# Kernel optimization log

Measured on AMD Instinct MI355X. Metric: run time of the kernel, lower is better.

Reference implementation:

```python
import jax, jax.numpy as jnp
import numpy as np

N = 50000   # nodes
E = 512000  # edges
D = 64      # embedding_dim
L = 4       # num_layers
ATOM_DIMS = np.array([119, 5, 12, 12, 10, 6, 6, 2, 2])  # OGB atom feature vocab sizes
BOND_DIMS = np.array([5, 6, 2])                          # OGB bond feature vocab sizes


def _ln(x, g, b, eps=1e-5):
    m = x.mean(-1, keepdims=True)
    v = x.var(-1, keepdims=True)
    return (x - m) * jax.lax.rsqrt(v + eps) * g + b


def setup_inputs() -> dict:
    key = jax.random.key(0)
    ks = jax.random.split(key, 12)
    s = 0.05
    x = jax.random.randint(ks[0], (N, 9), 0, jnp.asarray(ATOM_DIMS)[None, :])
    edge_attr = jax.random.randint(ks[1], (E, 3), 0, jnp.asarray(BOND_DIMS)[None, :])
    edge_index = jax.random.randint(ks[2], (2, E), 0, N)
    # padded embedding tables: [n_feats, max_vocab, D]
    atom_emb = jax.random.normal(ks[3], (9, 119, D), jnp.float32) * s
    bond_emb = jax.random.normal(ks[4], (3, 6, D), jnp.float32) * s
    eps = jnp.zeros((L,), jnp.float32)  # GIN eps, init 0
    W1 = jax.random.normal(ks[5], (L, D, 2 * D), jnp.float32) * s
    b1 = jnp.zeros((L, 2 * D), jnp.float32)
    W2 = jax.random.normal(ks[6], (L, 2 * D, D), jnp.float32) * s
    b2 = jnp.zeros((L, D), jnp.float32)
    ln_g = jnp.ones((L, D), jnp.float32)
    ln_b = jnp.zeros((L, D), jnp.float32)
    Wu1 = jax.random.normal(ks[7], (L, 3 * D, 3 * D), jnp.float32) * s
    bu1 = jnp.zeros((L, 3 * D), jnp.float32)
    ug = jnp.ones((L, 3 * D), jnp.float32)
    ub = jnp.zeros((L, 3 * D), jnp.float32)
    Wu2 = jax.random.normal(ks[8], (L, 3 * D, D), jnp.float32) * s
    bu2 = jnp.zeros((L, D), jnp.float32)
    return dict(x=x, edge_attr=edge_attr, edge_index=edge_index,
                atom_emb=atom_emb, bond_emb=bond_emb, eps=eps,
                W1=W1, b1=b1, W2=W2, b2=b2, ln_g=ln_g, ln_b=ln_b,
                Wu1=Wu1, bu1=bu1, ug=ug, ub=ub, Wu2=Wu2, bu2=bu2)


def reference(x, edge_attr, edge_index, atom_emb, bond_emb, eps,
              W1, b1, W2, b2, ln_g, ln_b, Wu1, bu1, ug, ub, Wu2, bu2):
    # Atom/Bond encoders: sum of per-column categorical embeddings
    node = atom_emb[jnp.arange(9)[None, :], x].sum(axis=1)       # [N, D]
    edge = bond_emb[jnp.arange(3)[None, :], edge_attr].sum(axis=1)  # [E, D]
    src, dst = edge_index[0], edge_index[1]
    for l in range(L):
        # MyGINConv (GINE): aggregate relu(x_src + e) at dst, mlp((1+eps)x + agg)
        msg = jax.nn.relu(node[src] + edge)                      # [E, D]
        agg = jax.ops.segment_sum(msg, dst, num_segments=N)      # [N, D]
        h = (1.0 + eps[l]) * node + agg
        h = jax.nn.relu(h @ W1[l] + b1[l]) @ W2[l] + b2[l]       # conv MLP
        h = _ln(h, ln_g[l], ln_b[l])                             # batch_norms[l] (LayerNorm)
        node = jax.nn.relu(h) + node                             # dropout=identity (eval) + residual
        # SparseEdgeUpdateLayer (residual=True)
        cat = jnp.concatenate([node[src], node[dst], edge], axis=-1)  # [E, 3D]
        m = _ln(cat @ Wu1[l] + bu1[l], ug[l], ub[l])
        edge = jax.nn.relu(m) @ Wu2[l] + bu2[l] + edge
    return node, edge
```

## Files before the change

kernel.cpp:

```cpp
#include <hip/hip_runtime.h>
#include <hip/hip_bf16.h>


#define GIN_N 50000
#define GIN_E 512000

typedef __attribute__((ext_vector_type(8))) short short8;
typedef __attribute__((ext_vector_type(4))) short short4v;
typedef __attribute__((ext_vector_type(4))) float f32x4;
typedef unsigned short u16;

__device__ __forceinline__ u16 bf16r(float x) {
    unsigned u = __builtin_bit_cast(unsigned, x);
    u += 0x7fffu + ((u >> 16) & 1u);
    return (u16)(u >> 16);
}
__device__ __forceinline__ float bf16f(u16 h) {
    unsigned u = ((unsigned)h) << 16;
    return __builtin_bit_cast(float, u);
}

__global__ __launch_bounds__(256) void zero_f32(float* __restrict__ p, int n) {
    int i = blockIdx.x * 256 + threadIdx.x;
    if (i < n) p[i] = 0.f;
}
__global__ __launch_bounds__(256) void zero_i32(int* __restrict__ p, int n) {
    int i = blockIdx.x * 256 + threadIdx.x;
    if (i < n) p[i] = 0;
}

__global__ __launch_bounds__(256) void atom_encode(const int* __restrict__ x,
        const float* __restrict__ emb, float* __restrict__ node, int N) {
    int idx = blockIdx.x * 256 + threadIdx.x;
    int n = idx >> 6, lane = idx & 63;
    if (n >= N) return;
    float s = 0.f;
#pragma unroll
    for (int f = 0; f < 9; ++f) {
        int v = x[n * 9 + f];
        s += emb[(f * 119 + v) * 64 + lane];
    }
    node[(size_t)n * 64 + lane] = s;
}

__global__ __launch_bounds__(256) void csr_hist(const int* __restrict__ dst,
                                                int* __restrict__ deg, int E) {
    int e = blockIdx.x * 256 + threadIdx.x;
    if (e < E) atomicAdd(&deg[dst[e]], 1);
}
__global__ __launch_bounds__(1024) void csr_scan(const int* __restrict__ deg,
                                                 int* __restrict__ cursor, int N) {
    __shared__ int ps[1024];
    const int t = threadIdx.x;
    const int chunk = (N + 1023) / 1024;
    const int base = t * chunk;
    int s = 0;
    for (int i = 0; i < chunk; ++i) {
        int idx = base + i;
        if (idx < N) s += deg[idx];
    }
    ps[t] = s;
    __syncthreads();
    for (int off = 1; off < 1024; off <<= 1) {
        int v = (t >= off) ? ps[t - off] : 0;
        __syncthreads();
        ps[t] += v;
        __syncthreads();
    }
    int run = ps[t] - s;
    for (int i = 0; i < chunk; ++i) {
        int idx = base + i;
        if (idx < N) { cursor[idx] = run; run += deg[idx]; }
    }
}
__global__ __launch_bounds__(256) void csr_fill(const int* __restrict__ src,
        const int* __restrict__ dst, int* __restrict__ cursor,
        int* __restrict__ perm, int* __restrict__ srcS, int* __restrict__ dstS,
        int E) {
    int e = blockIdx.x * 256 + threadIdx.x;
    if (e < E) {
        int d = dst[e];
        int pos = atomicAdd(&cursor[d], 1);
        perm[pos] = e;
        srcS[pos] = src[e];
        dstS[pos] = d;
    }
}

__global__ __launch_bounds__(256) void bond_encode_seg(
        const int* __restrict__ ea, const float* __restrict__ emb,
        u16* __restrict__ edgeB, const int* __restrict__ perm,
        const int* __restrict__ srcS, const int* __restrict__ dstS,
        const float* __restrict__ node, float* __restrict__ agg) {
    __shared__ float msgF[64][66];
    __shared__ int dstL[64];
    const int t = threadIdx.x, w = t >> 6, lane = t & 63;
    const int tile = (blockIdx.x & 7) * (gridDim.x >> 3) + (blockIdx.x >> 3);
    const long eB = (long)tile * 64;

    if (t < 64) dstL[t] = dstS[eB + t];
#pragma unroll 1
    for (int i = 0; i < 16; ++i) {
        int r = w * 16 + i;
        long e = eB + r;
        int pe = perm[e];
        float s = 0.f;
#pragma unroll
        for (int f = 0; f < 3; ++f) {
            int v = ea[pe * 3 + f];
            s += emb[(f * 6 + v) * 64 + lane];
        }
        edgeB[(size_t)e * 64 + lane] = bf16r(s);
        int si = srcS[e];
        msgF[r][lane] = fmaxf(node[(size_t)si * 64 + lane] + s, 0.f);
    }
    __syncthreads();
    const int colR = t & 63;
    const int h = t >> 6;
    float acc = 0.f;
#pragma unroll 1
    for (int r = h * 16; r < h * 16 + 16; ++r) {
        acc += msgF[r][colR];
        if (r == h * 16 + 15 || dstL[r + 1] != dstL[r]) {
            unsafeAtomicAdd(&agg[(size_t)dstL[r] * 64 + colR], acc);
            acc = 0.f;
        }
    }
}

__global__ __launch_bounds__(256) void pack_b1(const float* __restrict__ W,
        u16* __restrict__ out, int K, int Nc, int F) {
    int tid = blockIdx.x * 256 + threadIdx.x;
    int lane = tid & 63;
    int frag = (tid >> 6) % F;
    int layer = tid / (F * 64);
    int tpr = Nc / 16;
    int ks = frag / tpr, tt = frag % tpr;
    int k0 = ks * 32 + ((lane >> 4) << 3);
    int col = tt * 16 + (lane & 15);
    const float* w = W + (size_t)layer * K * Nc;
    u16* o = out + ((size_t)layer * F + frag) * 512 + (size_t)lane * 8;
#pragma unroll
    for (int j = 0; j < 8; ++j) o[j] = bf16r(w[(size_t)(k0 + j) * Nc + col]);
}
__global__ __launch_bounds__(256) void pack_b2(const float* __restrict__ W,
        u16* __restrict__ out, int K, int Nc, int F) {
    int tid = blockIdx.x * 256 + threadIdx.x;
    int lane = tid & 63;
    int frag = (tid >> 6) % F;
    int layer = tid / (F * 64);
    int tpr = Nc / 16;
    int ks = frag / tpr, tt = frag % tpr;
    int k0 = ks * 32 + ((lane >> 4) << 3);
    int col = tt * 16 + (lane & 15);
    const float* w = W + (size_t)layer * K * Nc;
    u16* o = out + ((size_t)layer * F + frag) * 1024 + (size_t)lane * 8;
#pragma unroll
    for (int j = 0; j < 8; ++j) {
        float v = w[(size_t)(k0 + j) * Nc + col];
        u16 hi = bf16r(v);
        o[j] = hi;
        o[512 + j] = bf16r(v - bf16f(hi));
    }
}

__global__ __launch_bounds__(256, 2) void node_mlp(
        float* __restrict__ node, u16* __restrict__ nodeB,
        float* __restrict__ agg,
        const float* __restrict__ epsArr, int l,
        const u16* __restrict__ pw1, const u16* __restrict__ pw2,
        const float* __restrict__ b1, const float* __restrict__ b2,
        const float* __restrict__ lng, const float* __restrict__ lnb, int N) {
    __shared__ u16 xH[64][72], xL[64][72];
    __shared__ u16 hH[64][136], hL[64][136];
    __shared__ float pS[4][64], pS2[4][64], lnM[64], lnR[64];
    const int t = threadIdx.x, w = t >> 6, lane = t & 63;
    const int g = lane >> 4, c0 = lane & 15;
    const float epf = 1.f + epsArr[l];

#pragma unroll
    for (int i = 0; i < 16; ++i) {
        int r = w * 16 + i;
        int n = blockIdx.x * 64 + r;
        float x = 0.f;
        if (n < N) {
            size_t o = (size_t)n * 64 + lane;
            x = epf * node[o] + agg[o];
            agg[o] = 0.f;
        }
        u16 h = bf16r(x);
        xH[r][lane] = h;
        xL[r][lane] = bf16r(x - bf16f(h));
    }
    __syncthreads();

    f32x4 a1[4][2];
#pragma unroll
    for (int sp = 0; sp < 4; ++sp)
#pragma unroll
        for (int lt = 0; lt < 2; ++lt) a1[sp][lt] = (f32x4)0.f;
#pragma unroll
    for (int ks = 0; ks < 2; ++ks) {
        short8 aH[4], aL[4];
#pragma unroll
        for (int sp = 0; sp < 4; ++sp) {
            aH[sp] = *(const short8*)&xH[sp * 16 + c0][ks * 32 + g * 8];
            aL[sp] = *(const short8*)&xL[sp * 16 + c0][ks * 32 + g * 8];
        }
#pragma unroll
        for (int lt = 0; lt < 2; ++lt) {
            const u16* p = pw1 + (size_t)(ks * 8 + w * 2 + lt) * 1024 + (size_t)lane * 8;
            short8 bH = *(const short8*)p;
            short8 bL = *(const short8*)(p + 512);
#pragma unroll
            for (int sp = 0; sp < 4; ++sp) {
                a1[sp][lt] = __builtin_amdgcn_mfma_f32_16x16x32_bf16(aH[sp], bH, a1[sp][lt], 0, 0, 0);
                a1[sp][lt] = __builtin_amdgcn_mfma_f32_16x16x32_bf16(aH[sp], bL, a1[sp][lt], 0, 0, 0);
                a1[sp][lt] = __builtin_amdgcn_mfma_f32_16x16x32_bf16(aL[sp], bH, a1[sp][lt], 0, 0, 0);
            }
        }
    }
#pragma unroll
    for (int lt = 0; lt < 2; ++lt) {
        int col = w * 32 + lt * 16 + c0;
        float bias = b1[col];
#pragma unroll
        for (int sp = 0; sp < 4; ++sp)
#pragma unroll
            for (int rg = 0; rg < 4; ++rg) {
                int r = sp * 16 + g * 4 + rg;
                float v = fmaxf(a1[sp][lt][rg] + bias, 0.f);
                u16 h = bf16r(v);
                hH[r][col] = h;
                hL[r][col] = bf16r(v - bf16f(h));
            }
    }
    __syncthreads();

    f32x4 a2[4];
#pragma unroll
    for (int sp = 0; sp < 4; ++sp) a2[sp] = (f32x4)0.f;
#pragma unroll
    for (int ks = 0; ks < 4; ++ks) {
        const u16* p = pw2 + (size_t)(ks * 4 + w) * 1024 + (size_t)lane * 8;
        short8 bH = *(const short8*)p;
        short8 bL = *(const short8*)(p + 512);
#pragma unroll
        for (int sp = 0; sp < 4; ++sp) {
            short8 aH = *(const short8*)&hH[sp * 16 + c0][ks * 32 + g * 8];
            short8 aL = *(const short8*)&hL[sp * 16 + c0][ks * 32 + g * 8];
            a2[sp] = __builtin_amdgcn_mfma_f32_16x16x32_bf16(aH, bH, a2[sp], 0, 0, 0);
            a2[sp] = __builtin_amdgcn_mfma_f32_16x16x32_bf16(aH, bL, a2[sp], 0, 0, 0);
            a2[sp] = __builtin_amdgcn_mfma_f32_16x16x32_bf16(aL, bH, a2[sp], 0, 0, 0);
        }
    }
    float bias2 = b2[w * 16 + c0];
    float s1v[4][4], s2v[4][4];
#pragma unroll
    for (int sp = 0; sp < 4; ++sp)
#pragma unroll
        for (int rg = 0; rg < 4; ++rg) {
            float v = a2[sp][rg] + bias2;
            a2[sp][rg] = v;
            s1v[sp][rg] = v;
            s2v[sp][rg] = v * v;
        }
#pragma unroll
    for (int off = 1; off < 16; off <<= 1)
#pragma unroll
        for (int sp = 0; sp < 4; ++sp)
#pragma unroll
            for (int rg = 0; rg < 4; ++rg) {
                s1v[sp][rg] += __shfl_xor(s1v[sp][rg], off);
                s2v[sp][rg] += __shfl_xor(s2v[sp][rg], off);
            }
    if (c0 == 0) {
#pragma unroll
        for (int sp = 0; sp < 4; ++sp)
#pragma unroll
            for (int rg = 0; rg < 4; ++rg) {
                int r = sp * 16 + g * 4 + rg;
                pS[w][r] = s1v[sp][rg];
                pS2[w][r] = s2v[sp][rg];
            }
    }
    __syncthreads();
    if (t < 64) {
        float a = pS[0][t] + pS[1][t] + pS[2][t] + pS[3][t];
        float b = pS2[0][t] + pS2[1][t] + pS2[2][t] + pS2[3][t];
        float mean = a * (1.f / 64.f);
        float var = b * (1.f / 64.f) - mean * mean;
        lnM[t] = mean;
        lnR[t] = rsqrtf(var + 1e-5f);
    }
    __syncthreads();

    int col = w * 16 + c0;
    float gg = lng[col], bc = lnb[col];
#pragma unroll
    for (int sp = 0; sp < 4; ++sp)
#pragma unroll
        for (int rg = 0; rg < 4; ++rg) {
            int r = sp * 16 + g * 4 + rg;
            int n = blockIdx.x * 64 + r;
            if (n < N) {
                size_t o = (size_t)n * 64 + col;
                float y = (a2[sp][rg] - lnM[r]) * lnR[r] * gg + bc;
                float out = fmaxf(y, 0.f) + node[o];
                node[o] = out;
                nodeB[o] = bf16r(out);
            }
        }
}

template <bool SCATTER>
__global__ __launch_bounds__(256, 4) void edge_update_v9(
        const int* __restrict__ src, const int* __restrict__ dst,
        const int* __restrict__ perm,
        const float* __restrict__ node, const u16* __restrict__ nodeB,
        u16* __restrict__ edgeB, float* __restrict__ edgeF,
        float* __restrict__ agg,
        const u16* __restrict__ pb1, const u16* __restrict__ pb2,
        const float* __restrict__ bu1, const float* __restrict__ ug,
        const float* __restrict__ ub, const float* __restrict__ bu2) {
    __shared__ u16 cat[64][200];
    __shared__ float pS[4][64], pS2[4][64];
    __shared__ float lnM[64], lnR[64];
    __shared__ int dstL[64], srcL[64];
    const int t = threadIdx.x, w = t >> 6, lane = t & 63;
    const int g = lane >> 4, c0 = lane & 15;
    const int tile = (blockIdx.x & 7) * (gridDim.x >> 3) + (blockIdx.x >> 3);
    const long eB = (long)tile * 64;

    if (t < 64) { dstL[t] = dst[eB + t]; srcL[t] = src[eB + t]; }
#pragma unroll
    for (int i = 0; i < 16; ++i) {
        int r = w * 16 + i;
        long ge = eB + r;
        int s = src[ge], d = dst[ge];
        cat[r][lane]      = nodeB[(size_t)s * 64 + lane];
        cat[r][64 + lane] = nodeB[(size_t)d * 64 + lane];
    }
    {
        const u16* eTile = edgeB + (size_t)eB * 64;
#pragma unroll
        for (int q = 0; q < 4; ++q) {
            int gi = t + q * 256;
            int r = gi >> 4, c4 = (gi & 15) * 4;
            *(short4v*)&cat[r][128 + c4] = *(const short4v*)(eTile + gi * 4);
        }
    }
    __syncthreads();

    u16 eold16[16];
#pragma unroll
    for (int sp = 0; sp < 4; ++sp)
#pragma unroll
        for (int rg = 0; rg < 4; ++rg)
            eold16[sp * 4 + rg] = cat[sp * 16 + g * 4 + rg][128 + w * 16 + c0];

    f32x4 acc[4][3];
#pragma unroll
    for (int sp = 0; sp < 4; ++sp)
#pragma unroll
        for (int lt = 0; lt < 3; ++lt) acc[sp][lt] = (f32x4)0.f;
#pragma unroll
    for (int ks = 0; ks < 6; ++ks) {
        short8 a[4];
#pragma unroll
        for (int sp = 0; sp < 4; ++sp)
            a[sp] = *(const short8*)&cat[sp * 16 + c0][ks * 32 + g * 8];
#pragma unroll
        for (int lt = 0; lt < 3; ++lt) {
            const u16* p = pb1 + (size_t)(ks * 12 + w * 3 + lt) * 512 + (size_t)lane * 8;
            short8 b = *(const short8*)p;
#pragma unroll
            for (int sp = 0; sp < 4; ++sp)
                acc[sp][lt] = __builtin_amdgcn_mfma_f32_16x16x32_bf16(a[sp], b, acc[sp][lt], 0, 0, 0);
        }
    }

    float bs[3];
#pragma unroll
    for (int lt = 0; lt < 3; ++lt) bs[lt] = bu1[w * 48 + lt * 16 + c0];
    float s1v[4][4], s2v[4][4];
#pragma unroll
    for (int sp = 0; sp < 4; ++sp)
#pragma unroll
        for (int rg = 0; rg < 4; ++rg) { s1v[sp][rg] = 0.f; s2v[sp][rg] = 0.f; }
#pragma unroll
    for (int sp = 0; sp < 4; ++sp)
#pragma unroll
        for (int lt = 0; lt < 3; ++lt)
#pragma unroll
            for (int rg = 0; rg < 4; ++rg) {
                float v = acc[sp][lt][rg] + bs[lt];
                acc[sp][lt][rg] = v;
                s1v[sp][rg] += v;
                s2v[sp][rg] += v * v;
            }
#pragma unroll
    for (int off = 1; off < 16; off <<= 1)
#pragma unroll
        for (int sp = 0; sp < 4; ++sp)
#pragma unroll
            for (int rg = 0; rg < 4; ++rg) {
                s1v[sp][rg] += __shfl_xor(s1v[sp][rg], off);
                s2v[sp][rg] += __shfl_xor(s2v[sp][rg], off);
            }
    if (c0 == 0) {
#pragma unroll
        for (int sp = 0; sp < 4; ++sp)
#pragma unroll
            for (int rg = 0; rg < 4; ++rg) {
                int r = sp * 16 + g * 4 + rg;
                pS[w][r] = s1v[sp][rg];
                pS2[w][r] = s2v[sp][rg];
            }
    }
    __syncthreads();
    if (t < 64) {
        float a = pS[0][t] + pS[1][t] + pS[2][t] + pS[3][t];
        float b = pS2[0][t] + pS2[1][t] + pS2[2][t] + pS2[3][t];
        float mean = a * (1.f / 192.f);
        float var = b * (1.f / 192.f) - mean * mean;
        lnM[t] = mean;
        lnR[t] = rsqrtf(var + 1e-5f);
    }
    __syncthreads();

#pragma unroll
    for (int lt = 0; lt < 3; ++lt) {
        int col = w * 48 + lt * 16 + c0;
        float gg = ug[col], bb = ub[col];
#pragma unroll
        for (int sp = 0; sp < 4; ++sp)
#pragma unroll
            for (int rg = 0; rg < 4; ++rg) {
                int r = sp * 16 + g * 4 + rg;
                float v = (acc[sp][lt][rg] - lnM[r]) * lnR[r] * gg + bb;
                cat[r][col] = bf16r(fmaxf(v, 0.f));
            }
    }
    __syncthreads();

    f32x4 a2[4];
#pragma unroll
    for (int sp = 0; sp < 4; ++sp) a2[sp] = (f32x4)0.f;
#pragma unroll
    for (int ks = 0; ks < 6; ++ks) {
        const u16* p = pb2 + (size_t)(ks * 4 + w) * 512 + (size_t)lane * 8;
        short8 b = *(const short8*)p;
#pragma unroll
        for (int sp = 0; sp < 4; ++sp) {
            short8 a = *(const short8*)&cat[sp * 16 + c0][ks * 32 + g * 8];
            a2[sp] = __builtin_amdgcn_mfma_f32_16x16x32_bf16(a, b, a2[sp], 0, 0, 0);
        }
    }
    __syncthreads();

    float* msgF = (float*)&cat[0][0];
    const int col = w * 16 + c0;
    const float bb2 = bu2[col];
#pragma unroll
    for (int sp = 0; sp < 4; ++sp)
#pragma unroll
        for (int rg = 0; rg < 4; ++rg) {
            int r = sp * 16 + g * 4 + rg;
            long ge = eB + r;
            float eNew = a2[sp][rg] + bb2 + bf16f(eold16[sp * 4 + rg]);
            if (SCATTER) {
                edgeB[(size_t)ge * 64 + col] = bf16r(eNew);
                float msg = fmaxf(node[(size_t)srcL[r] * 64 + col] + eNew, 0.f);
                msgF[r * 66 + col] = msg;
            } else {
                edgeF[(size_t)perm[ge] * 64 + col] = eNew;
            }
        }

    if (SCATTER) {
        __syncthreads();
        const int colR = t & 63;
        const int h = t >> 6;
        float accm = 0.f;
#pragma unroll 1
        for (int r = h * 16; r < h * 16 + 16; ++r) {
            accm += msgF[r * 66 + colR];
            if (r == h * 16 + 15 || dstL[r + 1] != dstL[r]) {
                unsafeAtomicAdd(&agg[(size_t)dstL[r] * 64 + colR], accm);
                accm = 0.f;
            }
        }
    }
}

extern "C" void kernel_launch(void* const* d_in, const int* in_sizes, int n_in,
                              void* d_out, int out_size, void* d_ws, size_t ws_size,
                              hipStream_t stream) {
    const int*   x         = (const int*)d_in[0];
    const int*   edge_attr = (const int*)d_in[1];
    const int*   edge_index= (const int*)d_in[2];
    const float* atom_emb  = (const float*)d_in[3];
    const float* bond_emb  = (const float*)d_in[4];
    const float* eps       = (const float*)d_in[5];
    const float* W1        = (const float*)d_in[6];
    const float* b1        = (const float*)d_in[7];
    const float* W2        = (const float*)d_in[8];
    const float* b2        = (const float*)d_in[9];
    const float* ln_g      = (const float*)d_in[10];
    const float* ln_b      = (const float*)d_in[11];
    const float* Wu1       = (const float*)d_in[12];
    const float* bu1       = (const float*)d_in[13];
    const float* ug        = (const float*)d_in[14];
    const float* ub        = (const float*)d_in[15];
    const float* Wu2       = (const float*)d_in[16];
    const float* bu2       = (const float*)d_in[17];

    const int N = GIN_N, E = GIN_E;
    const int* src = edge_index;
    const int* dst = edge_index + E;

    float* node  = (float*)d_out;
    float* edgeF = (float*)d_out + (size_t)N * 64;

    char* ws = (char*)d_ws;
    float* agg   = (float*)ws;  ws += (size_t)N * 64 * 4;
    u16*   nodeB = (u16*)ws;    ws += (size_t)N * 64 * 2;
    u16*   edgeB = (u16*)ws;    ws += (size_t)E * 64 * 2;
    int*   perm  = (int*)ws;    ws += (size_t)E * 4;
    int*   srcS  = (int*)ws;    ws += (size_t)E * 4;
    int*   dstS  = (int*)ws;    ws += (size_t)E * 4;
    int*   deg   = (int*)ws;    ws += (size_t)N * 4;
    int*   cursor= (int*)ws;    ws += (size_t)(N + 1) * 4;
    u16* pb1     = (u16*)ws;    ws += (size_t)4 * 72 * 512 * 2;
    u16* pb2     = (u16*)ws;    ws += (size_t)4 * 24 * 512 * 2;
    u16* pw1     = (u16*)ws;    ws += (size_t)4 * 16 * 1024 * 2;
    u16* pw2     = (u16*)ws;    ws += (size_t)4 * 16 * 1024 * 2;

    pack_b1<<<(4 * 72 * 64) / 256, 256, 0, stream>>>(Wu1, pb1, 192, 192, 72);
    pack_b1<<<(4 * 24 * 64) / 256, 256, 0, stream>>>(Wu2, pb2, 192, 64, 24);
    pack_b2<<<(4 * 16 * 64) / 256, 256, 0, stream>>>(W1, pw1, 64, 128, 16);
    pack_b2<<<(4 * 16 * 64) / 256, 256, 0, stream>>>(W2, pw2, 128, 64, 16);

    zero_i32<<<(N + 255) / 256, 256, 0, stream>>>(deg, N);
    csr_hist<<<E / 256, 256, 0, stream>>>(dst, deg, E);
    csr_scan<<<1, 1024, 0, stream>>>(deg, cursor, N);
    csr_fill<<<E / 256, 256, 0, stream>>>(src, dst, cursor, perm, srcS, dstS, E);

    atom_encode<<<(N * 64 + 255) / 256, 256, 0, stream>>>(x, atom_emb, node, N);
    zero_f32<<<(N * 64) / 256, 256, 0, stream>>>(agg, N * 64);
    bond_encode_seg<<<E / 64, 256, 0, stream>>>(edge_attr, bond_emb,
        edgeB, perm, srcS, dstS, node, agg);

    const int nodeBlocks = (N + 63) / 64;
    for (int l = 0; l < 4; ++l) {
        node_mlp<<<nodeBlocks, 256, 0, stream>>>(node, nodeB, agg, eps, l,
            pw1 + (size_t)l * 16 * 1024, pw2 + (size_t)l * 16 * 1024,
            b1 + (size_t)l * 128, b2 + (size_t)l * 64,
            ln_g + (size_t)l * 64, ln_b + (size_t)l * 64, N);
        if (l < 3)
            edge_update_v9<true><<<E / 64, 256, 0, stream>>>(srcS, dstS, perm,
                node, nodeB, edgeB, edgeF, agg,
                pb1 + (size_t)l * 72 * 512, pb2 + (size_t)l * 24 * 512,
                bu1 + (size_t)l * 192,
                ug + (size_t)l * 192, ub + (size_t)l * 192,
                bu2 + (size_t)l * 64);
        else
            edge_update_v9<false><<<E / 64, 256, 0, stream>>>(srcS, dstS, perm,
                node, nodeB, edgeB, edgeF, agg,
                pb1 + (size_t)l * 72 * 512, pb2 + (size_t)l * 24 * 512,
                bu1 + (size_t)l * 192,
                ug + (size_t)l * 192, ub + (size_t)l * 192,
                bu2 + (size_t)l * 64);
    }
}
```

Baseline: 959.5 us.

## Replace atomic scatter aggregation with CSR gather over materialized messages

Edge kernels now write per-edge relu messages in dst-sorted order to a buffer (aliasing the edge output), and node_mlp sums each node's contiguous message range via a CSR rowptr instead of reading an atomically accumulated agg buffer. This removes the float atomics, the agg zeroing and its reset, plus the shared-memory segment reduction. In exchange each layer writes and re-reads a full E×64 fp32 message array, greatly increasing memory traffic, and node_mlp's load phase becomes a serial variable-length gather.

```diff
diff --git a/kernel.cpp b/kernel.cpp
--- a/kernel.cpp
+++ b/kernel.cpp
@@ -20,10 +20,6 @@
     return __builtin_bit_cast(float, u);
 }
 
-__global__ __launch_bounds__(256) void zero_f32(float* __restrict__ p, int n) {
-    int i = blockIdx.x * 256 + threadIdx.x;
-    if (i < n) p[i] = 0.f;
-}
 __global__ __launch_bounds__(256) void zero_i32(int* __restrict__ p, int n) {
     int i = blockIdx.x * 256 + threadIdx.x;
     if (i < n) p[i] = 0;
@@ -49,7 +45,7 @@
     if (e < E) atomicAdd(&deg[dst[e]], 1);
 }
 __global__ __launch_bounds__(1024) void csr_scan(const int* __restrict__ deg,
-                                                 int* __restrict__ cursor, int N) {
+        int* __restrict__ rowptr, int* __restrict__ cursor, int N, int E) {
     __shared__ int ps[1024];
     const int t = threadIdx.x;
     const int chunk = (N + 1023) / 1024;
@@ -70,8 +66,9 @@
     int run = ps[t] - s;
     for (int i = 0; i < chunk; ++i) {
         int idx = base + i;
-        if (idx < N) { cursor[idx] = run; run += deg[idx]; }
-    }
+        if (idx < N) { rowptr[idx] = run; cursor[idx] = run; run += deg[idx]; }
+    }
+    if (t == 1023) rowptr[N] = E;
 }
 __global__ __launch_bounds__(256) void csr_fill(const int* __restrict__ src,
         const int* __restrict__ dst, int* __restrict__ cursor,
@@ -87,45 +84,24 @@
     }
 }
 
-__global__ __launch_bounds__(256) void bond_encode_seg(
+__global__ __launch_bounds__(256) void bond_encode_sorted(
         const int* __restrict__ ea, const float* __restrict__ emb,
-        u16* __restrict__ edgeB, const int* __restrict__ perm,
-        const int* __restrict__ srcS, const int* __restrict__ dstS,
-        const float* __restrict__ node, float* __restrict__ agg) {
-    __shared__ float msgF[64][66];
-    __shared__ int dstL[64];
-    const int t = threadIdx.x, w = t >> 6, lane = t & 63;
-    const int tile = (blockIdx.x & 7) * (gridDim.x >> 3) + (blockIdx.x >> 3);
-    const long eB = (long)tile * 64;
-
-    if (t < 64) dstL[t] = dstS[eB + t];
-#pragma unroll 1
-    for (int i = 0; i < 16; ++i) {
-        int r = w * 16 + i;
-        long e = eB + r;
-        int pe = perm[e];
-        float s = 0.f;
-#pragma unroll
-        for (int f = 0; f < 3; ++f) {
-            int v = ea[pe * 3 + f];
-            s += emb[(f * 6 + v) * 64 + lane];
-        }
-        edgeB[(size_t)e * 64 + lane] = bf16r(s);
-        int si = srcS[e];
-        msgF[r][lane] = fmaxf(node[(size_t)si * 64 + lane] + s, 0.f);
-    }
-    __syncthreads();
-    const int colR = t & 63;
-    const int h = t >> 6;
-    float acc = 0.f;
-#pragma unroll 1
-    for (int r = h * 16; r < h * 16 + 16; ++r) {
-        acc += msgF[r][colR];
-        if (r == h * 16 + 15 || dstL[r + 1] != dstL[r]) {
-            unsafeAtomicAdd(&agg[(size_t)dstL[r] * 64 + colR], acc);
-            acc = 0.f;
-        }
-    }
+        u16* __restrict__ edgeB, float* __restrict__ msg,
+        const int* __restrict__ perm, const int* __restrict__ srcS,
+        const float* __restrict__ node, int E) {
+    int idx = blockIdx.x * 256 + threadIdx.x;
+    int e = idx >> 6, lane = idx & 63;
+    if (e >= E) return;
+    int pe = perm[e];
+    float s = 0.f;
+#pragma unroll
+    for (int f = 0; f < 3; ++f) {
+        int v = ea[pe * 3 + f];
+        s += emb[(f * 6 + v) * 64 + lane];
+    }
+    edgeB[(size_t)e * 64 + lane] = bf16r(s);
+    int si = srcS[e];
+    msg[(size_t)e * 64 + lane] = fmaxf(node[(size_t)si * 64 + lane] + s, 0.f);
 }
 
 __global__ __launch_bounds__(256) void pack_b1(const float* __restrict__ W,
@@ -166,7 +142,7 @@
 
 __global__ __launch_bounds__(256, 2) void node_mlp(
         float* __restrict__ node, u16* __restrict__ nodeB,
-        float* __restrict__ agg,
+        const float* __restrict__ msg, const int* __restrict__ rowptr,
         const float* __restrict__ epsArr, int l,
         const u16* __restrict__ pw1, const u16* __restrict__ pw2,
         const float* __restrict__ b1, const float* __restrict__ b2,
@@ -178,15 +154,24 @@
     const int g = lane >> 4, c0 = lane & 15;
     const float epf = 1.f + epsArr[l];
 
-#pragma unroll
+#pragma unroll 1
     for (int i = 0; i < 16; ++i) {
         int r = w * 16 + i;
         int n = blockIdx.x * 64 + r;
         float x = 0.f;
         if (n < N) {
+            int jb = rowptr[n], je = rowptr[n + 1];
+            float a0 = 0.f, a1 = 0.f, a2v = 0.f, a3 = 0.f;
+            int j = jb;
+            for (; j + 3 < je; j += 4) {
+                a0  += msg[(size_t)j * 64 + lane];
+                a1  += msg[(size_t)(j + 1) * 64 + lane];
+                a2v += msg[(size_t)(j + 2) * 64 + lane];
+                a3  += msg[(size_t)(j + 3) * 64 + lane];
+            }
+            for (; j < je; ++j) a0 += msg[(size_t)j * 64 + lane];
             size_t o = (size_t)n * 64 + lane;
-            x = epf * node[o] + agg[o];
-            agg[o] = 0.f;
+            x = epf * node[o] + ((a0 + a1) + (a2v + a3));
         }
         u16 h = bf16r(x);
         xH[r][lane] = h;
@@ -313,26 +298,25 @@
         }
 }
 
-template <bool SCATTER>
-__global__ __launch_bounds__(256, 4) void edge_update_v9(
+template <bool LAST>
+__global__ __launch_bounds__(256, 4) void edge_update_v11(
         const int* __restrict__ src, const int* __restrict__ dst,
         const int* __restrict__ perm,
         const float* __restrict__ node, const u16* __restrict__ nodeB,
-        u16* __restrict__ edgeB, float* __restrict__ edgeF,
-        float* __restrict__ agg,
+        u16* __restrict__ edgeB, float* __restrict__ msgOrEdgeF,
         const u16* __restrict__ pb1, const u16* __restrict__ pb2,
         const float* __restrict__ bu1, const float* __restrict__ ug,
         const float* __restrict__ ub, const float* __restrict__ bu2) {
     __shared__ u16 cat[64][200];
     __shared__ float pS[4][64], pS2[4][64];
     __shared__ float lnM[64], lnR[64];
-    __shared__ int dstL[64], srcL[64];
+    __shared__ int srcL[64];
     const int t = threadIdx.x, w = t >> 6, lane = t & 63;
     const int g = lane >> 4, c0 = lane & 15;
     const int tile = (blockIdx.x & 7) * (gridDim.x >> 3) + (blockIdx.x >> 3);
     const long eB = (long)tile * 64;
 
-    if (t < 64) { dstL[t] = dst[eB + t]; srcL[t] = src[eB + t]; }
+    if (t < 64) srcL[t] = src[eB + t];
 #pragma unroll
     for (int i = 0; i < 16; ++i) {
         int r = w * 16 + i;
@@ -457,9 +441,7 @@
             a2[sp] = __builtin_amdgcn_mfma_f32_16x16x32_bf16(a, b, a2[sp], 0, 0, 0);
         }
     }
-    __syncthreads();
-
-    float* msgF = (float*)&cat[0][0];
+
     const int col = w * 16 + c0;
     const float bb2 = bu2[col];
 #pragma unroll
@@ -469,29 +451,14 @@
             int r = sp * 16 + g * 4 + rg;
             long ge = eB + r;
             float eNew = a2[sp][rg] + bb2 + bf16f(eold16[sp * 4 + rg]);
-            if (SCATTER) {
+            if (!LAST) {
                 edgeB[(size_t)ge * 64 + col] = bf16r(eNew);
-                float msg = fmaxf(node[(size_t)srcL[r] * 64 + col] + eNew, 0.f);
-                msgF[r * 66 + col] = msg;
+                float m = fmaxf(node[(size_t)srcL[r] * 64 + col] + eNew, 0.f);
+                msgOrEdgeF[(size_t)ge * 64 + col] = m;
             } else {
-                edgeF[(size_t)perm[ge] * 64 + col] = eNew;
-            }
-        }
-
-    if (SCATTER) {
-        __syncthreads();
-        const int colR = t & 63;
-        const int h = t >> 6;
-        float accm = 0.f;
-#pragma unroll 1
-        for (int r = h * 16; r < h * 16 + 16; ++r) {
-            accm += msgF[r * 66 + colR];
-            if (r == h * 16 + 15 || dstL[r + 1] != dstL[r]) {
-                unsafeAtomicAdd(&agg[(size_t)dstL[r] * 64 + colR], accm);
-                accm = 0.f;
-            }
-        }
-    }
+                msgOrEdgeF[(size_t)perm[ge] * 64 + col] = eNew;
+            }
+        }
 }
 
 extern "C" void kernel_launch(void* const* d_in, const int* in_sizes, int n_in,
@@ -520,18 +487,18 @@
     const int* src = edge_index;
     const int* dst = edge_index + E;
 
-    float* node  = (float*)d_out;
-    float* edgeF = (float*)d_out + (size_t)N * 64;
+    float* node = (float*)d_out;
+    float* msg  = (float*)d_out + (size_t)N * 64;
 
     char* ws = (char*)d_ws;
-    float* agg   = (float*)ws;  ws += (size_t)N * 64 * 4;
     u16*   nodeB = (u16*)ws;    ws += (size_t)N * 64 * 2;
     u16*   edgeB = (u16*)ws;    ws += (size_t)E * 64 * 2;
     int*   perm  = (int*)ws;    ws += (size_t)E * 4;
     int*   srcS  = (int*)ws;    ws += (size_t)E * 4;
     int*   dstS  = (int*)ws;    ws += (size_t)E * 4;
     int*   deg   = (int*)ws;    ws += (size_t)N * 4;
-    int*   cursor= (int*)ws;    ws += (size_t)(N + 1) * 4;
+    int*   rowptr= (int*)ws;    ws += (size_t)(N + 1) * 4;
+    int*   cursor= (int*)ws;    ws += (size_t)N * 4;
     u16* pb1     = (u16*)ws;    ws += (size_t)4 * 72 * 512 * 2;
     u16* pb2     = (u16*)ws;    ws += (size_t)4 * 24 * 512 * 2;
     u16* pw1     = (u16*)ws;    ws += (size_t)4 * 16 * 1024 * 2;
@@ -544,30 +511,29 @@
 
     zero_i32<<<(N + 255) / 256, 256, 0, stream>>>(deg, N);
     csr_hist<<<E / 256, 256, 0, stream>>>(dst, deg, E);
-    csr_scan<<<1, 1024, 0, stream>>>(deg, cursor, N);
+    csr_scan<<<1, 1024, 0, stream>>>(deg, rowptr, cursor, N, E);
     csr_fill<<<E / 256, 256, 0, stream>>>(src, dst, cursor, perm, srcS, dstS, E);
 
     atom_encode<<<(N * 64 + 255) / 256, 256, 0, stream>>>(x, atom_emb, node, N);
-    zero_f32<<<(N * 64) / 256, 256, 0, stream>>>(agg, N * 64);
-    bond_encode_seg<<<E / 64, 256, 0, stream>>>(edge_attr, bond_emb,
-        edgeB, perm, srcS, dstS, node, agg);
+    bond_encode_sorted<<<(E * 64) / 256, 256, 0, stream>>>(edge_attr, bond_emb,
+        edgeB, msg, perm, srcS, node, E);
 
     const int nodeBlocks = (N + 63) / 64;
     for (int l = 0; l < 4; ++l) {
-        node_mlp<<<nodeBlocks, 256, 0, stream>>>(node, nodeB, agg, eps, l,
+        node_mlp<<<nodeBlocks, 256, 0, stream>>>(node, nodeB, msg, rowptr, eps, l,
             pw1 + (size_t)l * 16 * 1024, pw2 + (size_t)l * 16 * 1024,
             b1 + (size_t)l * 128, b2 + (size_t)l * 64,
             ln_g + (size_t)l * 64, ln_b + (size_t)l * 64, N);
         if (l < 3)
-            edge_update_v9<true><<<E / 64, 256, 0, stream>>>(srcS, dstS, perm,
-                node, nodeB, edgeB, edgeF, agg,
+            edge_update_v11<false><<<E / 64, 256, 0, stream>>>(srcS, dstS, perm,
+                node, nodeB, edgeB, msg,
                 pb1 + (size_t)l * 72 * 512, pb2 + (size_t)l * 24 * 512,
                 bu1 + (size_t)l * 192,
                 ug + (size_t)l * 192, ub + (size_t)l * 192,
                 bu2 + (size_t)l * 64);
         else
-            edge_update_v9<false><<<E / 64, 256, 0, stream>>>(srcS, dstS, perm,
-                node, nodeB, edgeB, edgeF, agg,
+            edge_update_v11<true><<<E / 64, 256, 0, stream>>>(srcS, dstS, perm,
+                node, nodeB, edgeB, msg,
                 pb1 + (size_t)l * 72 * 512, pb2 + (size_t)l * 24 * 512,
                 bu1 + (size_t)l * 192,
                 ug + (size_t)l * 192, ub + (size_t)l * 192,
```

Result: slower. 1.199 ms (+25.0%).
